# Kernel optimization log

Hardware: AMD Instinct MI355X
Metric: run time of the kernel (lower is better)

The kernel has to match this reference:

```python
import jax, jax.numpy as jnp
import numpy as np
from jax import lax


def conv2d(x, w, b=None, stride=1, pad=0):
    y = lax.conv_general_dilated(x, w, (stride, stride), [(pad, pad), (pad, pad)],
                                 dimension_numbers=('NCHW', 'OIHW', 'NCHW'))
    if b is not None:
        y = y + b[None, :, None, None]
    return y


def bilinear_resize_ac(S, Ho, Wo):
    # F.interpolate(..., mode='bilinear', align_corners=True)
    B, C, H, W = S.shape
    ys = jnp.linspace(0.0, H - 1.0, Ho)
    xs = jnp.linspace(0.0, W - 1.0, Wo)
    y0 = jnp.floor(ys).astype(jnp.int32); y1 = jnp.minimum(y0 + 1, H - 1); wy = ys - y0
    x0 = jnp.floor(xs).astype(jnp.int32); x1 = jnp.minimum(x0 + 1, W - 1); wx = xs - x0
    Sy = S[:, :, y0, :] * (1 - wy)[None, None, :, None] + S[:, :, y1, :] * wy[None, None, :, None]
    return Sy[:, :, :, x0] * (1 - wx)[None, None, None, :] + Sy[:, :, :, x1] * wx[None, None, None, :]


def deform_conv(x, offset, weight, bias=None, mask=None, stride=1, pad=1, dil=1):
    # (Modulated) deformable conv, deformable_groups=1; DCNv2 semantics:
    # offset channels are (dy, dx) pairs per kernel tap; zero padding outside.
    B, C, H, W = x.shape
    O, Ci, kh, kw = weight.shape
    K = kh * kw
    Ho, Wo = offset.shape[2], offset.shape[3]
    off = offset.reshape(B, K, 2, Ho, Wo)
    kyy, kxx = jnp.meshgrid(jnp.arange(kh) * dil, jnp.arange(kw) * dil, indexing='ij')
    kyy = kyy.reshape(K).astype(x.dtype); kxx = kxx.reshape(K).astype(x.dtype)
    base_y = (jnp.arange(Ho) * stride - pad).astype(x.dtype)
    base_x = (jnp.arange(Wo) * stride - pad).astype(x.dtype)
    py = base_y[None, None, :, None] + kyy[None, :, None, None] + off[:, :, 0]  # [B,K,Ho,Wo]
    px = base_x[None, None, None, :] + kxx[None, :, None, None] + off[:, :, 1]
    y0 = jnp.floor(py); x0 = jnp.floor(px)
    dy = py - y0; dx = px - x0
    y0i = y0.astype(jnp.int32); x0i = x0.astype(jnp.int32)
    xf = x.reshape(B, C, H * W)

    def corner(yi, xi, w):
        valid = (yi >= 0) & (yi <= H - 1) & (xi >= 0) & (xi <= W - 1)
        yc = jnp.clip(yi, 0, H - 1); xc = jnp.clip(xi, 0, W - 1)
        idx = (yc * W + xc).reshape(B, -1)  # [B, K*Ho*Wo]
        g = jax.vmap(lambda f, i: f[:, i])(xf, idx)  # [B, C, K*Ho*Wo]
        g = g.reshape(B, C, K, Ho, Wo)
        return g * (w * valid.astype(x.dtype))[:, None]

    s = (corner(y0i, x0i, (1 - dy) * (1 - dx))
         + corner(y0i, x0i + 1, (1 - dy) * dx)
         + corner(y0i + 1, x0i, dy * (1 - dx))
         + corner(y0i + 1, x0i + 1, dy * dx))  # [B,C,K,Ho,Wo]
    if mask is not None:
        s = s * mask[:, None]  # [B,1,K,Ho,Wo]
    out = jnp.einsum('bckhw,ock->bohw', s, weight.reshape(O, Ci, K))
    if bias is not None:
        out = out + bias[None, :, None, None]
    return out


def setup_inputs():
    key = jax.random.key(0)
    ks = jax.random.split(key, 16)
    B, Cin, Cout, H, W = 8, 256, 256, 64, 64

    def n(k, shape, s):
        return jax.random.normal(k, shape, jnp.float32) * s

    return {
        'x': jax.random.normal(ks[0], (B, Cin, H, W), jnp.float32),
        'S': jax.random.normal(ks[1], (B, 3, 128, 128), jnp.float32),
        'sp_w1': n(ks[2], (64, 3, 3, 3), 0.2), 'sp_b1': jnp.zeros(64), 'sp_s1': jnp.ones(64) + n(ks[3], (64,), 0.05), 'sp_o1': n(ks[3], (64,), 0.05),
        'sp_w2': n(ks[4], (64, 64, 3, 3), 0.05), 'sp_b2': jnp.zeros(64), 'sp_s2': jnp.ones(64) + n(ks[5], (64,), 0.05), 'sp_o2': n(ks[5], (64,), 0.05),
        'sp_w3': n(ks[6], (64, 64, 3, 3), 0.05), 'sp_b3': jnp.zeros(64), 'sp_s3': jnp.ones(64) + n(ks[7], (64,), 0.05), 'sp_o3': n(ks[7], (64,), 0.05),
        'off_w': n(ks[8], (18, 64, 3, 3), 0.05), 'off_b': jnp.zeros(18),
        'dc_off_w': n(ks[9], (18, 64, 3, 3), 0.05), 'dc_off_b': jnp.zeros(18),
        'dc_w': n(ks[10], (64, 64, 3, 3), 0.04),
        'm_w': n(ks[11], (9, 64, 1, 1), 0.1), 'm_b': jnp.zeros(9),
        'weight': n(ks[12], (Cout, Cin, 3, 3), 0.02), 'bias': jnp.zeros(Cout),
    }


def reference(x, S, sp_w1, sp_b1, sp_s1, sp_o1, sp_w2, sp_b2, sp_s2, sp_o2,
              sp_w3, sp_b3, sp_s3, sp_o3, off_w, off_b, dc_off_w, dc_off_b,
              dc_w, m_w, m_b, weight, bias):
    H, W = x.shape[2], x.shape[3]
    Si = bilinear_resize_ac(S, H, W)
    h = jax.nn.relu(conv2d(Si, sp_w1, sp_b1, 1, 1) * sp_s1[None, :, None, None] + sp_o1[None, :, None, None])
    h = jax.nn.relu(conv2d(h, sp_w2, sp_b2, 1, 1) * sp_s2[None, :, None, None] + sp_o2[None, :, None, None])
    h = jax.nn.relu(conv2d(h, sp_w3, sp_b3, 1, 1) * sp_s3[None, :, None, None] + sp_o3[None, :, None, None])
    offset = conv2d(h, off_w, off_b, 1, 1)                 # [B,18,H,W]
    dc_off = conv2d(h, dc_off_w, dc_off_b, 1, 1)           # internal offsets of weight_generator1 (DCNv1)
    feat = deform_conv(h, dc_off, dc_w, None, None, 1, 1, 1)
    mask = jax.nn.sigmoid(conv2d(feat, m_w, m_b, 1, 0))    # [B,9,H,W]
    return deform_conv(x, offset, weight, bias, mask, 1, 1, 1)
```

## Files before the change

kernel.cpp:

```cpp
#include <hip/hip_runtime.h>
#include <hip/hip_bf16.h>

typedef unsigned short u16;
typedef unsigned int u32;
typedef __attribute__((ext_vector_type(8))) short short8;
typedef __attribute__((ext_vector_type(4))) unsigned short ush4;
typedef __attribute__((ext_vector_type(16))) float f32x16;

#define OXT   0
#define OSI   (OXT + 8388608)
#define OA    (OSI + 98304)
#define OB    (OA + 2097152)
#define OC    (OB + 2097152)
#define OOFFS (OC + 2097152)
#define OMSK  (OOFFS + 1179648)
#define OWT   (OMSK + 294912)
#define OWSP1 (OWT + 589824)
#define OBSP1 (OWSP1 + 1728)
#define OWSP2 (OBSP1 + 64)
#define OBSP2 (OWSP2 + 36864)
#define OWSP3 (OBSP2 + 64)
#define OBSP3 (OWSP3 + 36864)
#define OWOFF (OBSP3 + 64)
#define OBOFF (OWOFF + 36864)
#define OWDC  (OBOFF + 64)

__device__ __forceinline__ u16 f2bf(float f) {
    __hip_bfloat16 hb = __float2bfloat16(f);
    return __builtin_bit_cast(u16, hb);
}
__device__ __forceinline__ float bf2f(u16 v) {
    return __builtin_bit_cast(float, (u32)v << 16);
}
__device__ __forceinline__ int sswz(int kg, int px) {
    return (px & ~7) | ((px ^ kg) & 7);
}

__device__ __forceinline__ void corner_tab_big(
    int tap, int pix0, int b, int gp,
    const float* __restrict__ offs, const float* __restrict__ maskb,
    int* car, float* cwr)
{
    int pix = pix0 + gp; int pib = pix & 4095;
    int y = pib >> 6, x = pib & 63;
    float offy = offs[(size_t)pix * 36 + tap * 2];
    float offx = offs[(size_t)pix * 36 + tap * 2 + 1];
    float m = maskb[(size_t)pix * 9 + tap];
    float py = (float)(y - 1 + tap / 3) + offy;
    float pxf = (float)(x - 1 + (tap % 3)) + offx;
    float fy = floorf(py), fx = floorf(pxf);
    int y0 = (int)fy, x0 = (int)fx;
    float dyf = py - fy, dxf = pxf - fx;
    #pragma unroll
    for (int j = 0; j < 4; j++) {
        float wj = ((j >> 1) ? dyf : 1.f - dyf) * ((j & 1) ? dxf : 1.f - dxf);
        int yy = y0 + (j >> 1), xx = x0 + (j & 1);
        bool valid = (yy >= 0 && yy < 64 && xx >= 0 && xx < 64);
        int yc = min(max(yy, 0), 63), xc = min(max(xx, 0), 63);
        car[j] = (b * 4096 + yc * 64 + xc) << 8;
        cwr[j] = valid ? wj * m : 0.f;
    }
}

__global__ __launch_bounds__(256) void prologue_k(
    const float* __restrict__ weight,
    const float* __restrict__ sp_w1, const float* __restrict__ sp_s1,
    const float* __restrict__ sp_w2, const float* __restrict__ sp_s2,
    const float* __restrict__ sp_w3, const float* __restrict__ sp_s3,
    const float* __restrict__ off_w, const float* __restrict__ dc_off_w,
    const float* __restrict__ dc_w,
    const float* __restrict__ sp_b1, const float* __restrict__ sp_o1,
    const float* __restrict__ sp_b2, const float* __restrict__ sp_o2,
    const float* __restrict__ sp_b3, const float* __restrict__ sp_o3,
    const float* __restrict__ off_b, const float* __restrict__ dc_off_b,
    const float* __restrict__ x, const float* __restrict__ S,
    float* __restrict__ ws)
{
    __shared__ float tile[64][65];
    int blk = blockIdx.x;
    int t = threadIdx.x;

    if (blk >= 4936) {
        int i = (blk - 4936) * 256 + t;
        if (i >= 8 * 64 * 64 * 3) return;
        int c = i % 3; int xq = (i / 3) & 63; int y = (i / 192) & 63; int b = i / 12288;
        const float sc = 127.0f / 63.0f;
        float sy = y * sc, sx = xq * sc;
        float fy = floorf(sy), fx = floorf(sx);
        int y0 = (int)fy, x0 = (int)fx;
        int y1 = min(y0 + 1, 127), x1 = min(x0 + 1, 127);
        float wy = sy - fy, wx = sx - fx;
        const float* Sb = S + (size_t)(b * 3 + c) * 16384;
        float v00 = Sb[y0 * 128 + x0], v01 = Sb[y0 * 128 + x1];
        float v10 = Sb[y1 * 128 + x0], v11 = Sb[y1 * 128 + x1];
        (ws + OSI)[i] = (v00 * (1.f - wy) + v10 * wy) * (1.f - wx)
                      + (v01 * (1.f - wy) + v11 * wy) * wx;
        return;
    }
    if (blk >= 2888) {
        int bb = blk - 2888;
        int chunk = bb & 3; int by = bb >> 2;
        int b = by >> 6; int y = by & 63;
        int c0 = chunk * 64;
        u16* xT = (u16*)(ws + OXT);
        for (int i = t; i < 4096; i += 256) {
            int ci = i >> 6, xi = i & 63;
            tile[ci][xi] = x[((b * 256 + c0 + ci) * 64 + y) * 64 + xi];
        }
        __syncthreads();
        for (int i = t; i < 4096; i += 256) {
            int xi = i >> 6, ci = i & 63;
            xT[((b * 64 + y) * 64 + xi) * 256 + c0 + ci] = f2bf(tile[ci][xi]);
        }
        return;
    }
    int i = blk * 256 + t;
    if (i < 589824) {
        int j = i & 7; int o = (i >> 3) & 255; int kg = i >> 11;
        int K = kg * 8 + j; int k = K >> 8; int c = K & 255;
        ((u16*)(ws + OWT))[i] = f2bf(weight[o * 2304 + c * 9 + k]);
        return;
    }
    i -= 589824;
    if (i < 1728) {
        int o = i & 63; int kc = i >> 6; int c = kc % 3; int k = kc / 3;
        ws[OWSP1 + i] = sp_w1[(o * 3 + c) * 9 + k] * sp_s1[o];
        return;
    }
    i -= 1728;
    if (i < 36864) {
        int e = i & 7; int o = (i >> 3) & 63; int kg = (i >> 9) & 7; int tp = i >> 12;
        ((u16*)(ws + OWSP2))[i] = f2bf(sp_w2[(o * 64 + kg * 8 + e) * 9 + tp] * sp_s2[o]);
        return;
    }
    i -= 36864;
    if (i < 36864) {
        int e = i & 7; int o = (i >> 3) & 63; int kg = (i >> 9) & 7; int tp = i >> 12;
        ((u16*)(ws + OWSP3))[i] = f2bf(sp_w3[(o * 64 + kg * 8 + e) * 9 + tp] * sp_s3[o]);
        return;
    }
    i -= 36864;
    if (i < 36864) {
        int e = i & 7; int o = (i >> 3) & 63; int kg = (i >> 9) & 7; int tp = i >> 12;
        int c = kg * 8 + e;
        float v = 0.f;
        if (o < 18) v = off_w[(o * 64 + c) * 9 + tp];
        else if (o < 36) v = dc_off_w[((o - 18) * 64 + c) * 9 + tp];
        ((u16*)(ws + OWOFF))[i] = f2bf(v);
        return;
    }
    i -= 36864;
    if (i < 36864) {
        int e = i & 7; int o = (i >> 3) & 63; int kg = (i >> 9) & 7; int tp = i >> 12;
        ((u16*)(ws + OWDC))[i] = f2bf(dc_w[(o * 64 + kg * 8 + e) * 9 + tp]);
        return;
    }
    i -= 36864;
    if (i < 64) { ws[OBSP1 + i] = sp_b1[i] * sp_s1[i] + sp_o1[i]; return; }
    i -= 64;
    if (i < 64) { ws[OBSP2 + i] = sp_b2[i] * sp_s2[i] + sp_o2[i]; return; }
    i -= 64;
    if (i < 64) { ws[OBSP3 + i] = sp_b3[i] * sp_s3[i] + sp_o3[i]; return; }
    i -= 64;
    if (i < 64) { ws[OBOFF + i] = (i < 18) ? off_b[i] : (i < 36 ? dc_off_b[i - 18] : 0.f); return; }
}

__global__ __launch_bounds__(256) void conv_in_k(const float* __restrict__ in,
                                                 const float* __restrict__ wt,
                                                 const float* __restrict__ bias,
                                                 u16* __restrict__ out)
{
    __shared__ float rows[3][66][3];
    int by = blockIdx.x; int b = by >> 6; int y = by & 63;
    int t = threadIdx.x;
    for (int i = t; i < 3 * 66 * 3; i += 256) {
        int r = i / 198; int rem = i - r * 198;
        int xi = rem / 3; int c = rem - xi * 3;
        int yy = y - 1 + r, xx = xi - 1;
        float v = 0.f;
        if (yy >= 0 && yy < 64 && xx >= 0 && xx < 64)
            v = in[(((b * 64 + yy) * 64 + xx) * 3) + c];
        rows[r][xi][c] = v;
    }
    __syncthreads();
    int o4 = (t & 15) * 4; int xg = t >> 4;
    float acc[4][4];
    #pragma unroll
    for (int oi = 0; oi < 4; oi++) {
        float bv = bias[o4 + oi];
        #pragma unroll
        for (int xi = 0; xi < 4; xi++) acc[oi][xi] = bv;
    }
    for (int k = 0; k < 9; k++) {
        int dy = k / 3, dx = k - 3 * (k / 3);
        for (int c = 0; c < 3; c++) {
            float4 w = *reinterpret_cast<const float4*>(&wt[(k * 3 + c) * 64 + o4]);
            #pragma unroll
            for (int xi = 0; xi < 4; xi++) {
                float iv = rows[dy][xg * 4 + xi + dx][c];
                acc[0][xi] = fmaf(w.x, iv, acc[0][xi]);
                acc[1][xi] = fmaf(w.y, iv, acc[1][xi]);
                acc[2][xi] = fmaf(w.z, iv, acc[2][xi]);
                acc[3][xi] = fmaf(w.w, iv, acc[3][xi]);
            }
        }
    }
    #pragma unroll
    for (int xi = 0; xi < 4; xi++) {
        int x = xg * 4 + xi;
        ush4 v;
        v.x = f2bf(fmaxf(acc[0][xi], 0.f));
        v.y = f2bf(fmaxf(acc[1][xi], 0.f));
        v.z = f2bf(fmaxf(acc[2][xi], 0.f));
        v.w = f2bf(fmaxf(acc[3][xi], 0.f));
        *reinterpret_cast<ush4*>(&out[((size_t)(by * 64 + x)) * 64 + o4]) = v;
    }
}

template <int MODE, bool RELU>
__global__ __launch_bounds__(256) void conv_mfma_k(const u16* __restrict__ in,
                                                   const u16* __restrict__ wm,
                                                   const float* __restrict__ bias,
                                                   u16* __restrict__ outH,
                                                   float* __restrict__ outF)
{
    __shared__ __attribute__((aligned(16))) char lds_h[3 * 66 * 128];
    __shared__ __attribute__((aligned(16))) u16 wtap[2][8][64][8];

    int t = threadIdx.x;
    int b = blockIdx.x >> 6; int y = blockIdx.x & 63;
    int pix0 = b * 4096 + y * 64;
    int wid = t >> 6, lane = t & 63;
    int lrow = lane & 31, lhi = lane >> 5;
    int o0 = (wid & 1) << 5;
    int px0 = (wid >> 1) << 5;
    int px = px0 + lrow;

    for (int i = t; i < 3 * 66 * 8; i += 256) {
        int r = i / 528; int rem = i - r * 528;
        int xi = rem >> 3; int g = rem & 7;
        int yy = y - 1 + r, xx = xi - 1;
        short8 v = {0,0,0,0,0,0,0,0};
        if (yy >= 0 && yy < 64 && xx >= 0 && xx < 64)
            v = *reinterpret_cast<const short8*>(&in[(size_t)((b * 4096 + yy * 64 + xx)) * 64 + g * 8]);
        int byte = (r * 66 + xi) * 128 + ((g * 16) ^ ((xi & 7) << 4));
        *reinterpret_cast<short8*>(lds_h + byte) = v;
    }
    {
        const char* gb = (const char*)(wm);
        char* lb = (char*)&wtap[0][0][0][0];
        #pragma unroll
        for (int i = 0; i < 2; i++) {
            int off = i * 4096 + wid * 1024;
            __builtin_amdgcn_global_load_lds(
                (const __attribute__((address_space(1))) void*)(gb + off + lane * 16),
                (__attribute__((address_space(3))) void*)(lb + off), 16, 0, 0);
        }
    }
    __syncthreads();

    f32x16 acc;
    #pragma unroll
    for (int r = 0; r < 16; r++) acc[r] = 0.f;

    #pragma unroll
    for (int tap = 0; tap < 9; tap++) {
        int cur = tap & 1, nxt = cur ^ 1;
        if (tap < 8) {
            const char* gb = (const char*)(wm + (size_t)(tap + 1) * 4096);
            char* lb = (char*)&wtap[nxt][0][0][0];
            #pragma unroll
            for (int i = 0; i < 2; i++) {
                int off = i * 4096 + wid * 1024;
                __builtin_amdgcn_global_load_lds(
                    (const __attribute__((address_space(1))) void*)(gb + off + lane * 16),
                    (__attribute__((address_space(3))) void*)(lb + off), 16, 0, 0);
            }
        }
        int dy = tap / 3, dx = tap - 3 * (tap / 3);
        int xi = px + dx;
        int rowbyte = (dy * 66 + xi) * 128;
        int swz = (xi & 7) << 4;
        #pragma unroll
        for (int ks = 0; ks < 4; ks++) {
            int kg = ks * 2 + lhi;
            short8 a0 = *reinterpret_cast<const short8*>(&wtap[cur][kg][o0 + lrow][0]);
            short8 b0 = *reinterpret_cast<const short8*>(lds_h + rowbyte + ((kg * 16) ^ swz));
            acc = __builtin_amdgcn_mfma_f32_32x32x16_bf16(a0, b0, acc, 0, 0, 0);
        }
        if (tap < 8) asm volatile("s_waitcnt vmcnt(0)" ::: "memory");
        __builtin_amdgcn_s_barrier();
    }
    __syncthreads();

    if (MODE == 0) {
        #pragma unroll
        for (int q = 0; q < 4; q++) {
            int ob = o0 + q * 8 + 4 * lhi;
            #pragma unroll
            for (int h = 0; h < 2; h++) {
                float v0 = acc[q * 4 + h * 2] + bias[ob + h * 2];
                float v1 = acc[q * 4 + h * 2 + 1] + bias[ob + h * 2 + 1];
                if (RELU) { v0 = fmaxf(v0, 0.f); v1 = fmaxf(v1, 0.f); }
                u32 pk = (u32)f2bf(v0) | ((u32)f2bf(v1) << 16);
                int byte = px * 128 + (((ob + h * 2) * 2) ^ ((px & 7) << 4));
                *reinterpret_cast<u32*>(lds_h + byte) = pk;
            }
        }
        __syncthreads();
        #pragma unroll
        for (int i = 0; i < 2; i++) {
            int cid = i * 256 + t;
            int p = cid >> 3, g = cid & 7;
            short8 v = *reinterpret_cast<const short8*>(lds_h + p * 128 + ((g * 16) ^ ((p & 7) << 4)));
            *reinterpret_cast<short8*>(&outH[(size_t)(pix0 + p) * 64 + g * 8]) = v;
        }
    } else {
        float* ltf = (float*)lds_h;
        #pragma unroll
        for (int r = 0; r < 16; r++) {
            int o = o0 + (r & 3) + ((r >> 2) << 3) + (lhi << 2);
            if (o < 36) ltf[px * 40 + o] = acc[r] + bias[o];
        }
        __syncthreads();
        for (int i = t; i < 576; i += 256) {
            int p = i / 9, q = i - 9 * (i / 9);
            float4 v = *reinterpret_cast<const float4*>(&ltf[p * 40 + q * 4]);
            *reinterpret_cast<float4*>(&outF[(size_t)(pix0 + p) * 36 + q * 4]) = v;
        }
    }
}

__global__ __launch_bounds__(512) void dconv_small_mfma(
    const u16* __restrict__ h, const float* __restrict__ offs,
    const u16* __restrict__ wdc, const float* __restrict__ m_w,
    const float* __restrict__ m_b, float* __restrict__ maskb)
{
    __shared__ __attribute__((aligned(16))) char smem[49152];
    u16 (*wtile)[8][64][8]  = (u16 (*)[8][64][8])smem;
    u16 (*stile)[8][128][8] = (u16 (*)[8][128][8])(smem + 16384);

    int t = threadIdx.x;
    int id = blockIdx.x;
    int blk = (id & 7) * 32 + (id >> 3);
    int pix0 = blk * 128;
    int b = pix0 >> 12;
    int wid = t >> 6, lane = t & 63;
    int lrow = lane & 31, lhi = lane >> 5;
    int o0 = (wid & 1) << 5;
    int px0 = (wid >> 1) << 5;
    int gp = t >> 2, gsub = t & 3;

    {
        const char* gb = (const char*)wdc;
        char* lb = (char*)&wtile[0][0][0][0];
        __builtin_amdgcn_global_load_lds(
            (const __attribute__((address_space(1))) void*)(gb + wid * 1024 + lane * 16),
            (__attribute__((address_space(3))) void*)(lb + wid * 1024), 16, 0, 0);
    }

    f32x16 acc;
    #pragma unroll
    for (int r = 0; r < 16; r++) acc[r] = 0.f;

    int car[4]; float cwr[4];

    for (int tap = 0; tap < 9; ++tap) {
        int cur = tap & 1, nxt = cur ^ 1;
        {
            int pix = pix0 + gp; int pib = pix & 4095;
            int y = pib >> 6, x = pib & 63;
            float offy = offs[(size_t)pix * 36 + 18 + tap * 2];
            float offx = offs[(size_t)pix * 36 + 18 + tap * 2 + 1];
            float py = (float)(y - 1 + tap / 3) + offy;
            float pxf = (float)(x - 1 + (tap % 3)) + offx;
            float fy = floorf(py), fx = floorf(pxf);
            int y0 = (int)fy, x0 = (int)fx;
            float dyf = py - fy, dxf = pxf - fx;
            #pragma unroll
            for (int j = 0; j < 4; j++) {
                float wj = ((j >> 1) ? dyf : 1.f - dyf) * ((j & 1) ? dxf : 1.f - dxf);
                int yy = y0 + (j >> 1), xx = x0 + (j & 1);
                bool valid = (yy >= 0 && yy < 64 && xx >= 0 && xx < 64);
                int yc = min(max(yy, 0), 63), xc = min(max(xx, 0), 63);
                car[j] = (b * 4096 + yc * 64 + xc) << 6;
                cwr[j] = valid ? wj : 0.f;
            }
        }
        int c = gsub << 4;
        float va[16];
        #pragma unroll
        for (int e = 0; e < 16; e++) va[e] = 0.f;
        #pragma unroll
        for (int j = 0; j < 4; j++) {
            float w = cwr[j];
            const u16* p = h + car[j] + c;
            short8 r0 = *reinterpret_cast<const short8*>(p);
            short8 r1 = *reinterpret_cast<const short8*>(p + 8);
            #pragma unroll
            for (int e = 0; e < 8; e++) {
                va[e]     = fmaf(w, bf2f((u16)r0[e]), va[e]);
                va[8 + e] = fmaf(w, bf2f((u16)r1[e]), va[8 + e]);
            }
        }
        short8 s0, s1;
        #pragma unroll
        for (int e = 0; e < 8; e++) { s0[e] = (short)f2bf(va[e]); s1[e] = (short)f2bf(va[8 + e]); }
        int kg0 = gsub * 2, kg1 = gsub * 2 + 1;
        *reinterpret_cast<short8*>(&stile[cur][kg0][sswz(kg0, gp)][0]) = s0;
        *reinterpret_cast<short8*>(&stile[cur][kg1][sswz(kg1, gp)][0]) = s1;

        asm volatile("s_waitcnt vmcnt(0) lgkmcnt(0)" ::: "memory");
        __builtin_amdgcn_s_barrier();

        #pragma unroll
        for (int ks = 0; ks < 4; ks++) {
            int kg = ks * 2 + lhi;
            short8 a0 = *reinterpret_cast<const short8*>(&wtile[cur][kg][o0 + lrow][0]);
            short8 b0 = *reinterpret_cast<const short8*>(&stile[cur][kg][sswz(kg, px0 + lrow)][0]);
            acc = __builtin_amdgcn_mfma_f32_32x32x16_bf16(a0, b0, acc, 0, 0, 0);
        }
        if (tap < 8) {
            const char* gb = (const char*)(wdc + (size_t)(tap + 1) * 4096);
            char* lb = (char*)&wtile[nxt][0][0][0];
            __builtin_amdgcn_global_load_lds(
                (const __attribute__((address_space(1))) void*)(gb + wid * 1024 + lane * 16),
                (__attribute__((address_space(3))) void*)(lb + wid * 1024), 16, 0, 0);
        }
    }

    __syncthreads();
    float* featl = (float*)smem;
    int pxl = px0 + lrow;
    #pragma unroll
    for (int r = 0; r < 16; r++) {
        int o = o0 + (r & 3) + ((r >> 2) << 3) + (lhi << 2);
        featl[pxl * 65 + o] = acc[r];
    }
    __syncthreads();
    if (t < 256) {
        int p = t >> 1, hh = t & 1;
        int pix = pix0 + p;
        const float* fr = &featl[p * 65];
        int j0 = hh ? 4 : 0, j1 = hh ? 9 : 4;
        for (int j = j0; j < j1; j++) {
            float a = m_b[j];
            #pragma unroll 8
            for (int cc = 0; cc < 64; cc++) a = fmaf(fr[cc], m_w[j * 64 + cc], a);
            maskb[(size_t)pix * 9 + j] = 1.f / (1.f + expf(-a));
        }
    }
}

__global__ __launch_bounds__(512) void dconv_big_mfma(
    const u16* __restrict__ xT, const float* __restrict__ offs,
    const float* __restrict__ maskb, const u16* __restrict__ wKg,
    const float* __restrict__ bias, float* __restrict__ out)
{
    __shared__ __attribute__((aligned(16))) u16 wtile[2][8][256][8];
    __shared__ __attribute__((aligned(16))) u16 stile[2][8][128][8];

    int t = threadIdx.x;
    int id = blockIdx.x;
    int blk = (id & 7) * 32 + (id >> 3);
    int pix0 = blk * 128;
    int b = pix0 >> 12, pib0 = pix0 & 4095;
    int wid = t >> 6, lane = t & 63;
    int lrow = lane & 31, lhi = lane >> 5;
    int o0 = (wid & 3) << 6;
    int px0 = (wid >> 2) << 6;
    int gp = t >> 2, gsub = t & 3;

    int car[4]; float cwr[4];
    short8 g[8];

    corner_tab_big(0, pix0, b, gp, offs, maskb, car, cwr);
    {
        int c = gsub << 4;
        #pragma unroll
        for (int j = 0; j < 4; j++) {
            const u16* p = xT + car[j] + c;
            g[j * 2]     = *reinterpret_cast<const short8*>(p);
            g[j * 2 + 1] = *reinterpret_cast<const short8*>(p + 8);
        }
    }
    {
        const char* gb = (const char*)wKg;
        char* lb = (char*)&wtile[0][0][0][0];
        #pragma unroll
        for (int i = 0; i < 4; i++) {
            int off = i * 8192 + wid * 1024;
            __builtin_amdgcn_global_load_lds(
                (const __attribute__((address_space(1))) void*)(gb + off + lane * 16),
                (__attribute__((address_space(3))) void*)(lb + off), 16, 0, 0);
        }
    }

    f32x16 acc[2][2];
    #pragma unroll
    for (int ao = 0; ao < 2; ao++)
        #pragma unroll
        for (int bp = 0; bp < 2; bp++)
            #pragma unroll
            for (int r = 0; r < 16; r++) acc[ao][bp][r] = 0.f;

    for (int kt = 0; kt < 36; ++kt) {
        int cur = kt & 1, nxt = cur ^ 1;

        float va[16];
        #pragma unroll
        for (int e = 0; e < 16; e++) va[e] = 0.f;
        #pragma unroll
        for (int j = 0; j < 4; j++) {
            float w = cwr[j];
            #pragma unroll
            for (int e = 0; e < 8; e++) {
                va[e]     = fmaf(w, bf2f((u16)g[j * 2][e]), va[e]);
                va[8 + e] = fmaf(w, bf2f((u16)g[j * 2 + 1][e]), va[8 + e]);
            }
        }
        short8 s0, s1;
        #pragma unroll
        for (int e = 0; e < 8; e++) { s0[e] = (short)f2bf(va[e]); s1[e] = (short)f2bf(va[8 + e]); }
        int kg0 = gsub * 2, kg1 = gsub * 2 + 1;
        *reinterpret_cast<short8*>(&stile[cur][kg0][sswz(kg0, gp)][0]) = s0;
        *reinterpret_cast<short8*>(&stile[cur][kg1][sswz(kg1, gp)][0]) = s1;

        if (kt < 35) {
            if (((kt + 1) & 3) == 0)
                corner_tab_big((kt + 1) >> 2, pix0, b, gp, offs, maskb, car, cwr);
            int c = (((kt + 1) & 3) << 6) + (gsub << 4);
            #pragma unroll
            for (int j = 0; j < 4; j++) {
                const u16* p = xT + car[j] + c;
                g[j * 2]     = *reinterpret_cast<const short8*>(p);
                g[j * 2 + 1] = *reinterpret_cast<const short8*>(p + 8);
            }
            asm volatile("s_waitcnt vmcnt(8) lgkmcnt(0)" ::: "memory");
        } else {
            asm volatile("s_waitcnt vmcnt(0) lgkmcnt(0)" ::: "memory");
        }
        __builtin_amdgcn_s_barrier();

        #pragma unroll
        for (int ks = 0; ks < 4; ks++) {
            int kg = ks * 2 + lhi;
            short8 a0 = *reinterpret_cast<const short8*>(&wtile[cur][kg][o0 + lrow][0]);
            short8 a1 = *reinterpret_cast<const short8*>(&wtile[cur][kg][o0 + 32 + lrow][0]);
            short8 b0 = *reinterpret_cast<const short8*>(&stile[cur][kg][sswz(kg, px0 + lrow)][0]);
            short8 b1 = *reinterpret_cast<const short8*>(&stile[cur][kg][sswz(kg, px0 + 32 + lrow)][0]);
            acc[0][0] = __builtin_amdgcn_mfma_f32_32x32x16_bf16(a0, b0, acc[0][0], 0, 0, 0);
            acc[0][1] = __builtin_amdgcn_mfma_f32_32x32x16_bf16(a0, b1, acc[0][1], 0, 0, 0);
            acc[1][0] = __builtin_amdgcn_mfma_f32_32x32x16_bf16(a1, b0, acc[1][0], 0, 0, 0);
            acc[1][1] = __builtin_amdgcn_mfma_f32_32x32x16_bf16(a1, b1, acc[1][1], 0, 0, 0);
        }
        if (kt < 35) {
            const char* gb = (const char*)(wKg + (size_t)(kt + 1) * 16384);
            char* lb = (char*)&wtile[nxt][0][0][0];
            #pragma unroll
            for (int i = 0; i < 4; i++) {
                int off = i * 8192 + wid * 1024;
                __builtin_amdgcn_global_load_lds(
                    (const __attribute__((address_space(1))) void*)(gb + off + lane * 16),
                    (__attribute__((address_space(3))) void*)(lb + off), 16, 0, 0);
            }
        }
    }

    #pragma unroll
    for (int ao = 0; ao < 2; ao++) {
        #pragma unroll
        for (int r = 0; r < 16; r++) {
            int o = o0 + ao * 32 + (r & 3) + ((r >> 2) << 3) + (lhi << 2);
            float bv = bias[o];
            size_t rowoff = ((size_t)(b * 256 + o) << 12) + pib0 + px0;
            out[rowoff + lrow] = acc[ao][0][r] + bv;
            out[rowoff + 32 + lrow] = acc[ao][1][r] + bv;
        }
    }
}

extern "C" void kernel_launch(void* const* d_in, const int* in_sizes, int n_in,
                              void* d_out, int out_size, void* d_ws, size_t ws_size,
                              hipStream_t stream)
{
    const float* x        = (const float*)d_in[0];
    const float* S        = (const float*)d_in[1];
    const float* sp_w1    = (const float*)d_in[2];
    const float* sp_b1    = (const float*)d_in[3];
    const float* sp_s1    = (const float*)d_in[4];
    const float* sp_o1    = (const float*)d_in[5];
    const float* sp_w2    = (const float*)d_in[6];
    const float* sp_b2    = (const float*)d_in[7];
    const float* sp_s2    = (const float*)d_in[8];
    const float* sp_o2    = (const float*)d_in[9];
    const float* sp_w3    = (const float*)d_in[10];
    const float* sp_b3    = (const float*)d_in[11];
    const float* sp_s3    = (const float*)d_in[12];
    const float* sp_o3    = (const float*)d_in[13];
    const float* off_w    = (const float*)d_in[14];
    const float* off_b    = (const float*)d_in[15];
    const float* dc_off_w = (const float*)d_in[16];
    const float* dc_off_b = (const float*)d_in[17];
    const float* dc_w     = (const float*)d_in[18];
    const float* m_w      = (const float*)d_in[19];
    const float* m_b      = (const float*)d_in[20];
    const float* weight   = (const float*)d_in[21];
    const float* bias     = (const float*)d_in[22];
    float* out = (float*)d_out;
    float* ws  = (float*)d_ws;

    u16*   xTb   = (u16*)(ws + OXT);
    float* Si    = ws + OSI;
    u16*   h1    = (u16*)(ws + OA);
    u16*   h2    = (u16*)(ws + OB);
    u16*   h3    = (u16*)(ws + OC);
    float* offsb = ws + OOFFS;
    float* maskb = ws + OMSK;

    prologue_k<<<5320, 256, 0, stream>>>(weight, sp_w1, sp_s1, sp_w2, sp_s2,
                                         sp_w3, sp_s3, off_w, dc_off_w, dc_w,
                                         sp_b1, sp_o1, sp_b2, sp_o2, sp_b3, sp_o3,
                                         off_b, dc_off_b, x, S, ws);
    conv_in_k<<<512, 256, 0, stream>>>(Si, ws + OWSP1, ws + OBSP1, h1);
    conv_mfma_k<0, true><<<512, 256, 0, stream>>>(h1, (const u16*)(ws + OWSP2),
                                                  ws + OBSP2, h2, nullptr);
    conv_mfma_k<0, true><<<512, 256, 0, stream>>>(h2, (const u16*)(ws + OWSP3),
                                                  ws + OBSP3, h3, nullptr);
    conv_mfma_k<1, false><<<512, 256, 0, stream>>>(h3, (const u16*)(ws + OWOFF),
                                                   ws + OBOFF, nullptr, offsb);
    dconv_small_mfma<<<256, 512, 0, stream>>>(h3, offsb, (const u16*)(ws + OWDC),
                                              m_w, m_b, maskb);
    dconv_big_mfma<<<256, 512, 0, stream>>>(xTb, offsb, maskb,
                                            (const u16*)(ws + OWT), bias, out);
}
```

Measured before the change: 132.0 us.

## Prefetch gathers across taps, triple-buffer conv weights, halve big deform-conv pixel tile

conv_mfma_k now keeps three weight-tap buffers and prefetches two taps ahead, waiting with a partial vmcnt so a weight load overlaps more compute. dconv_small_mfma computes the next tap's corner table and issues its bilinear gathers before the barrier, so gather latency overlaps the current tap's MFMAs. dconv_big_mfma shrinks each block's pixel tile from 128 to 64, launches twice as many blocks, and gives each wave 32 outputs by 64 pixels with fewer registers. The aim is better latency hiding and occupancy, at the cost of more LDS in the conv kernel and more weight-tile reloads across the extra blocks.

```diff
diff --git a/kernel.cpp b/kernel.cpp
--- a/kernel.cpp
+++ b/kernel.cpp
@@ -62,6 +62,30 @@
     }
 }
 
+__device__ __forceinline__ void corner_tab_small(
+    int tap, int pix0, int b, int gp,
+    const float* __restrict__ offs, int* car, float* cwr)
+{
+    int pix = pix0 + gp; int pib = pix & 4095;
+    int y = pib >> 6, x = pib & 63;
+    float offy = offs[(size_t)pix * 36 + 18 + tap * 2];
+    float offx = offs[(size_t)pix * 36 + 18 + tap * 2 + 1];
+    float py = (float)(y - 1 + tap / 3) + offy;
+    float pxf = (float)(x - 1 + (tap % 3)) + offx;
+    float fy = floorf(py), fx = floorf(pxf);
+    int y0 = (int)fy, x0 = (int)fx;
+    float dyf = py - fy, dxf = pxf - fx;
+    #pragma unroll
+    for (int j = 0; j < 4; j++) {
+        float wj = ((j >> 1) ? dyf : 1.f - dyf) * ((j & 1) ? dxf : 1.f - dxf);
+        int yy = y0 + (j >> 1), xx = x0 + (j & 1);
+        bool valid = (yy >= 0 && yy < 64 && xx >= 0 && xx < 64);
+        int yc = min(max(yy, 0), 63), xc = min(max(xx, 0), 63);
+        car[j] = (b * 4096 + yc * 64 + xc) << 6;
+        cwr[j] = valid ? wj : 0.f;
+    }
+}
+
 __global__ __launch_bounds__(256) void prologue_k(
     const float* __restrict__ weight,
     const float* __restrict__ sp_w1, const float* __restrict__ sp_s1,
@@ -225,7 +249,7 @@
                                                    float* __restrict__ outF)
 {
     __shared__ __attribute__((aligned(16))) char lds_h[3 * 66 * 128];
-    __shared__ __attribute__((aligned(16))) u16 wtap[2][8][64][8];
+    __shared__ __attribute__((aligned(16))) u16 wtap[3][8][64][8];
 
     int t = threadIdx.x;
     int b = blockIdx.x >> 6; int y = blockIdx.x & 63;
@@ -246,9 +270,10 @@
         int byte = (r * 66 + xi) * 128 + ((g * 16) ^ ((xi & 7) << 4));
         *reinterpret_cast<short8*>(lds_h + byte) = v;
     }
-    {
-        const char* gb = (const char*)(wm);
-        char* lb = (char*)&wtap[0][0][0][0];
+    #pragma unroll
+    for (int p = 0; p < 2; p++) {
+        const char* gb = (const char*)(wm + (size_t)p * 4096);
+        char* lb = (char*)&wtap[p][0][0][0];
         #pragma unroll
         for (int i = 0; i < 2; i++) {
             int off = i * 4096 + wid * 1024;
@@ -265,10 +290,11 @@
 
     #pragma unroll
     for (int tap = 0; tap < 9; tap++) {
-        int cur = tap & 1, nxt = cur ^ 1;
-        if (tap < 8) {
-            const char* gb = (const char*)(wm + (size_t)(tap + 1) * 4096);
-            char* lb = (char*)&wtap[nxt][0][0][0];
+        int cur = tap % 3;
+        if (tap < 7) {
+            int nb = (tap + 2) % 3;
+            const char* gb = (const char*)(wm + (size_t)(tap + 2) * 4096);
+            char* lb = (char*)&wtap[nb][0][0][0];
             #pragma unroll
             for (int i = 0; i < 2; i++) {
                 int off = i * 4096 + wid * 1024;
@@ -288,8 +314,11 @@
             short8 b0 = *reinterpret_cast<const short8*>(lds_h + rowbyte + ((kg * 16) ^ swz));
             acc = __builtin_amdgcn_mfma_f32_32x32x16_bf16(a0, b0, acc, 0, 0, 0);
         }
-        if (tap < 8) asm volatile("s_waitcnt vmcnt(0)" ::: "memory");
-        __builtin_amdgcn_s_barrier();
+        if (tap < 8) {
+            if (tap < 7) asm volatile("s_waitcnt vmcnt(2)" ::: "memory");
+            else         asm volatile("s_waitcnt vmcnt(0)" ::: "memory");
+            __builtin_amdgcn_s_barrier();
+        }
     }
     __syncthreads();
 
@@ -351,6 +380,19 @@
     int px0 = (wid >> 1) << 5;
     int gp = t >> 2, gsub = t & 3;
 
+    int car[4]; float cwr[4];
+    short8 g[8];
+
+    corner_tab_small(0, pix0, b, gp, offs, car, cwr);
+    {
+        int c = gsub << 4;
+        #pragma unroll
+        for (int j = 0; j < 4; j++) {
+            const u16* p = h + car[j] + c;
+            g[j * 2]     = *reinterpret_cast<const short8*>(p);
+            g[j * 2 + 1] = *reinterpret_cast<const short8*>(p + 8);
+        }
+    }
     {
         const char* gb = (const char*)wdc;
         char* lb = (char*)&wtile[0][0][0][0];
@@ -363,44 +405,19 @@
     #pragma unroll
     for (int r = 0; r < 16; r++) acc[r] = 0.f;
 
-    int car[4]; float cwr[4];
-
     for (int tap = 0; tap < 9; ++tap) {
         int cur = tap & 1, nxt = cur ^ 1;
-        {
-            int pix = pix0 + gp; int pib = pix & 4095;
-            int y = pib >> 6, x = pib & 63;
-            float offy = offs[(size_t)pix * 36 + 18 + tap * 2];
-            float offx = offs[(size_t)pix * 36 + 18 + tap * 2 + 1];
-            float py = (float)(y - 1 + tap / 3) + offy;
-            float pxf = (float)(x - 1 + (tap % 3)) + offx;
-            float fy = floorf(py), fx = floorf(pxf);
-            int y0 = (int)fy, x0 = (int)fx;
-            float dyf = py - fy, dxf = pxf - fx;
-            #pragma unroll
-            for (int j = 0; j < 4; j++) {
-                float wj = ((j >> 1) ? dyf : 1.f - dyf) * ((j & 1) ? dxf : 1.f - dxf);
-                int yy = y0 + (j >> 1), xx = x0 + (j & 1);
-                bool valid = (yy >= 0 && yy < 64 && xx >= 0 && xx < 64);
-                int yc = min(max(yy, 0), 63), xc = min(max(xx, 0), 63);
-                car[j] = (b * 4096 + yc * 64 + xc) << 6;
-                cwr[j] = valid ? wj : 0.f;
-            }
-        }
-        int c = gsub << 4;
+
         float va[16];
         #pragma unroll
         for (int e = 0; e < 16; e++) va[e] = 0.f;
         #pragma unroll
         for (int j = 0; j < 4; j++) {
             float w = cwr[j];
-            const u16* p = h + car[j] + c;
-            short8 r0 = *reinterpret_cast<const short8*>(p);
-            short8 r1 = *reinterpret_cast<const short8*>(p + 8);
             #pragma unroll
             for (int e = 0; e < 8; e++) {
-                va[e]     = fmaf(w, bf2f((u16)r0[e]), va[e]);
-                va[8 + e] = fmaf(w, bf2f((u16)r1[e]), va[8 + e]);
+                va[e]     = fmaf(w, bf2f((u16)g[j * 2][e]), va[e]);
+                va[8 + e] = fmaf(w, bf2f((u16)g[j * 2 + 1][e]), va[8 + e]);
             }
         }
         short8 s0, s1;
@@ -410,7 +427,19 @@
         *reinterpret_cast<short8*>(&stile[cur][kg0][sswz(kg0, gp)][0]) = s0;
         *reinterpret_cast<short8*>(&stile[cur][kg1][sswz(kg1, gp)][0]) = s1;
 
-        asm volatile("s_waitcnt vmcnt(0) lgkmcnt(0)" ::: "memory");
+        if (tap < 8) {
+            corner_tab_small(tap + 1, pix0, b, gp, offs, car, cwr);
+            int c = gsub << 4;
+            #pragma unroll
+            for (int j = 0; j < 4; j++) {
+                const u16* p = h + car[j] + c;
+                g[j * 2]     = *reinterpret_cast<const short8*>(p);
+                g[j * 2 + 1] = *reinterpret_cast<const short8*>(p + 8);
+            }
+            asm volatile("s_waitcnt vmcnt(8) lgkmcnt(0)" ::: "memory");
+        } else {
+            asm volatile("s_waitcnt vmcnt(0) lgkmcnt(0)" ::: "memory");
+        }
         __builtin_amdgcn_s_barrier();
 
         #pragma unroll
@@ -458,31 +487,27 @@
     const float* __restrict__ bias, float* __restrict__ out)
 {
     __shared__ __attribute__((aligned(16))) u16 wtile[2][8][256][8];
-    __shared__ __attribute__((aligned(16))) u16 stile[2][8][128][8];
+    __shared__ __attribute__((aligned(16))) u16 stile[2][8][64][8];
 
     int t = threadIdx.x;
     int id = blockIdx.x;
-    int blk = (id & 7) * 32 + (id >> 3);
-    int pix0 = blk * 128;
+    int blk = (id & 7) * 64 + (id >> 3);
+    int pix0 = blk * 64;
     int b = pix0 >> 12, pib0 = pix0 & 4095;
     int wid = t >> 6, lane = t & 63;
     int lrow = lane & 31, lhi = lane >> 5;
-    int o0 = (wid & 3) << 6;
-    int px0 = (wid >> 2) << 6;
-    int gp = t >> 2, gsub = t & 3;
+    int o0 = wid << 5;
+    int gp = t >> 3, gsub = t & 7;
 
     int car[4]; float cwr[4];
-    short8 g[8];
+    short8 g[4];
 
     corner_tab_big(0, pix0, b, gp, offs, maskb, car, cwr);
     {
-        int c = gsub << 4;
-        #pragma unroll
-        for (int j = 0; j < 4; j++) {
-            const u16* p = xT + car[j] + c;
-            g[j * 2]     = *reinterpret_cast<const short8*>(p);
-            g[j * 2 + 1] = *reinterpret_cast<const short8*>(p + 8);
-        }
+        int c = gsub << 3;
+        #pragma unroll
+        for (int j = 0; j < 4; j++)
+            g[j] = *reinterpret_cast<const short8*>(xT + car[j] + c);
     }
     {
         const char* gb = (const char*)wKg;
@@ -496,47 +521,37 @@
         }
     }
 
-    f32x16 acc[2][2];
-    #pragma unroll
-    for (int ao = 0; ao < 2; ao++)
-        #pragma unroll
-        for (int bp = 0; bp < 2; bp++)
-            #pragma unroll
-            for (int r = 0; r < 16; r++) acc[ao][bp][r] = 0.f;
+    f32x16 acc[2];
+    #pragma unroll
+    for (int fp = 0; fp < 2; fp++)
+        #pragma unroll
+        for (int r = 0; r < 16; r++) acc[fp][r] = 0.f;
 
     for (int kt = 0; kt < 36; ++kt) {
         int cur = kt & 1, nxt = cur ^ 1;
 
-        float va[16];
-        #pragma unroll
-        for (int e = 0; e < 16; e++) va[e] = 0.f;
+        float va[8];
+        #pragma unroll
+        for (int e = 0; e < 8; e++) va[e] = 0.f;
         #pragma unroll
         for (int j = 0; j < 4; j++) {
             float w = cwr[j];
             #pragma unroll
-            for (int e = 0; e < 8; e++) {
-                va[e]     = fmaf(w, bf2f((u16)g[j * 2][e]), va[e]);
-                va[8 + e] = fmaf(w, bf2f((u16)g[j * 2 + 1][e]), va[8 + e]);
-            }
-        }
-        short8 s0, s1;
-        #pragma unroll
-        for (int e = 0; e < 8; e++) { s0[e] = (short)f2bf(va[e]); s1[e] = (short)f2bf(va[8 + e]); }
-        int kg0 = gsub * 2, kg1 = gsub * 2 + 1;
-        *reinterpret_cast<short8*>(&stile[cur][kg0][sswz(kg0, gp)][0]) = s0;
-        *reinterpret_cast<short8*>(&stile[cur][kg1][sswz(kg1, gp)][0]) = s1;
+            for (int e = 0; e < 8; e++) va[e] = fmaf(w, bf2f((u16)g[j][e]), va[e]);
+        }
+        short8 s0;
+        #pragma unroll
+        for (int e = 0; e < 8; e++) s0[e] = (short)f2bf(va[e]);
+        *reinterpret_cast<short8*>(&stile[cur][gsub][sswz(gsub, gp)][0]) = s0;
 
         if (kt < 35) {
             if (((kt + 1) & 3) == 0)
                 corner_tab_big((kt + 1) >> 2, pix0, b, gp, offs, maskb, car, cwr);
-            int c = (((kt + 1) & 3) << 6) + (gsub << 4);
-            #pragma unroll
-            for (int j = 0; j < 4; j++) {
-                const u16* p = xT + car[j] + c;
-                g[j * 2]     = *reinterpret_cast<const short8*>(p);
-                g[j * 2 + 1] = *reinterpret_cast<const short8*>(p + 8);
-            }
-            asm volatile("s_waitcnt vmcnt(8) lgkmcnt(0)" ::: "memory");
+            int c = (((kt + 1) & 3) << 6) + (gsub << 3);
+            #pragma unroll
+            for (int j = 0; j < 4; j++)
+                g[j] = *reinterpret_cast<const short8*>(xT + car[j] + c);
+            asm volatile("s_waitcnt vmcnt(4) lgkmcnt(0)" ::: "memory");
         } else {
             asm volatile("s_waitcnt vmcnt(0) lgkmcnt(0)" ::: "memory");
         }
@@ -546,13 +561,10 @@
         for (int ks = 0; ks < 4; ks++) {
             int kg = ks * 2 + lhi;
             short8 a0 = *reinterpret_cast<const short8*>(&wtile[cur][kg][o0 + lrow][0]);
-            short8 a1 = *reinterpret_cast<const short8*>(&wtile[cur][kg][o0 + 32 + lrow][0]);
-            short8 b0 = *reinterpret_cast<const short8*>(&stile[cur][kg][sswz(kg, px0 + lrow)][0]);
-            short8 b1 = *reinterpret_cast<const short8*>(&stile[cur][kg][sswz(kg, px0 + 32 + lrow)][0]);
-            acc[0][0] = __builtin_amdgcn_mfma_f32_32x32x16_bf16(a0, b0, acc[0][0], 0, 0, 0);
-            acc[0][1] = __builtin_amdgcn_mfma_f32_32x32x16_bf16(a0, b1, acc[0][1], 0, 0, 0);
-            acc[1][0] = __builtin_amdgcn_mfma_f32_32x32x16_bf16(a1, b0, acc[1][0], 0, 0, 0);
-            acc[1][1] = __builtin_amdgcn_mfma_f32_32x32x16_bf16(a1, b1, acc[1][1], 0, 0, 0);
+            short8 b0 = *reinterpret_cast<const short8*>(&stile[cur][kg][sswz(kg, lrow)][0]);
+            short8 b1 = *reinterpret_cast<const short8*>(&stile[cur][kg][sswz(kg, 32 + lrow)][0]);
+            acc[0] = __builtin_amdgcn_mfma_f32_32x32x16_bf16(a0, b0, acc[0], 0, 0, 0);
+            acc[1] = __builtin_amdgcn_mfma_f32_32x32x16_bf16(a0, b1, acc[1], 0, 0, 0);
         }
         if (kt < 35) {
             const char* gb = (const char*)(wKg + (size_t)(kt + 1) * 16384);
@@ -568,14 +580,12 @@
     }
 
     #pragma unroll
-    for (int ao = 0; ao < 2; ao++) {
+    for (int fp = 0; fp < 2; fp++) {
         #pragma unroll
         for (int r = 0; r < 16; r++) {
-            int o = o0 + ao * 32 + (r & 3) + ((r >> 2) << 3) + (lhi << 2);
-            float bv = bias[o];
-            size_t rowoff = ((size_t)(b * 256 + o) << 12) + pib0 + px0;
-            out[rowoff + lrow] = acc[ao][0][r] + bv;
-            out[rowoff + 32 + lrow] = acc[ao][1][r] + bv;
+            int o = o0 + (r & 3) + ((r >> 2) << 3) + (lhi << 2);
+            size_t rowoff = ((size_t)(b * 256 + o) << 12) + pib0;
+            out[rowoff + fp * 32 + lrow] = acc[fp][r] + bias[o];
         }
     }
 }
@@ -631,6 +641,6 @@
                                                    ws + OBOFF, nullptr, offsb);
     dconv_small_mfma<<<256, 512, 0, stream>>>(h3, offsb, (const u16*)(ws + OWDC),
                                               m_w, m_b, maskb);
-    dconv_big_mfma<<<256, 512, 0, stream>>>(xTb, offsb, maskb,
+    dconv_big_mfma<<<512, 512, 0, stream>>>(xTb, offsb, maskb,
                                             (const u16*)(ws + OWT), bias, out);
 }
```

After: 137.6 us. +4.2%, slower.

## Preload all conv tap weights to LDS, double rows per block, prefetch deform gathers

Applied to the files above, without the earlier changes.

The 3x3 MFMA conv kernels now load all nine taps' weights into LDS up front, which removes the per-tap double-buffered weight loads and barriers. Each block now covers two output rows with 512 threads, so grid size halves. The small deformable conv likewise preloads all tap weights and software-pipelines the bilinear corner gathers, issuing the next tap's global loads before the MFMA of the current tap. The cost is much larger LDS per block, around 104KB in the small deform kernel, which reduces occupancy. The extra register-held gather data also adds pressure.

```diff
diff --git a/kernel.cpp b/kernel.cpp
--- a/kernel.cpp
+++ b/kernel.cpp
@@ -62,6 +62,30 @@
     }
 }
 
+__device__ __forceinline__ void corner_tab_small(
+    int tap, int pix0, int b, int gp,
+    const float* __restrict__ offs, int* car, float* cwr)
+{
+    int pix = pix0 + gp; int pib = pix & 4095;
+    int y = pib >> 6, x = pib & 63;
+    float offy = offs[(size_t)pix * 36 + 18 + tap * 2];
+    float offx = offs[(size_t)pix * 36 + 18 + tap * 2 + 1];
+    float py = (float)(y - 1 + tap / 3) + offy;
+    float pxf = (float)(x - 1 + (tap % 3)) + offx;
+    float fy = floorf(py), fx = floorf(pxf);
+    int y0 = (int)fy, x0 = (int)fx;
+    float dyf = py - fy, dxf = pxf - fx;
+    #pragma unroll
+    for (int j = 0; j < 4; j++) {
+        float wj = ((j >> 1) ? dyf : 1.f - dyf) * ((j & 1) ? dxf : 1.f - dxf);
+        int yy = y0 + (j >> 1), xx = x0 + (j & 1);
+        bool valid = (yy >= 0 && yy < 64 && xx >= 0 && xx < 64);
+        int yc = min(max(yy, 0), 63), xc = min(max(xx, 0), 63);
+        car[j] = (b * 4096 + yc * 64 + xc) << 6;
+        cwr[j] = valid ? wj : 0.f;
+    }
+}
+
 __global__ __launch_bounds__(256) void prologue_k(
     const float* __restrict__ weight,
     const float* __restrict__ sp_w1, const float* __restrict__ sp_s1,
@@ -218,28 +242,29 @@
 }
 
 template <int MODE, bool RELU>
-__global__ __launch_bounds__(256) void conv_mfma_k(const u16* __restrict__ in,
+__global__ __launch_bounds__(512) void conv_mfma_k(const u16* __restrict__ in,
                                                    const u16* __restrict__ wm,
                                                    const float* __restrict__ bias,
                                                    u16* __restrict__ outH,
                                                    float* __restrict__ outF)
 {
-    __shared__ __attribute__((aligned(16))) char lds_h[3 * 66 * 128];
-    __shared__ __attribute__((aligned(16))) u16 wtap[2][8][64][8];
+    __shared__ __attribute__((aligned(16))) char lds_h[4 * 66 * 128];
+    __shared__ __attribute__((aligned(16))) u16 wtap[9][8][64][8];
 
     int t = threadIdx.x;
-    int b = blockIdx.x >> 6; int y = blockIdx.x & 63;
-    int pix0 = b * 4096 + y * 64;
+    int b = blockIdx.x >> 5; int y0 = (blockIdx.x & 31) * 2;
+    int pix0 = b * 4096 + y0 * 64;
     int wid = t >> 6, lane = t & 63;
     int lrow = lane & 31, lhi = lane >> 5;
     int o0 = (wid & 1) << 5;
     int px0 = (wid >> 1) << 5;
     int px = px0 + lrow;
-
-    for (int i = t; i < 3 * 66 * 8; i += 256) {
+    int ry_l = px >> 6, xc = px & 63;
+
+    for (int i = t; i < 4 * 66 * 8; i += 512) {
         int r = i / 528; int rem = i - r * 528;
         int xi = rem >> 3; int g = rem & 7;
-        int yy = y - 1 + r, xx = xi - 1;
+        int yy = y0 - 1 + r, xx = xi - 1;
         short8 v = {0,0,0,0,0,0,0,0};
         if (yy >= 0 && yy < 64 && xx >= 0 && xx < 64)
             v = *reinterpret_cast<const short8*>(&in[(size_t)((b * 4096 + yy * 64 + xx)) * 64 + g * 8]);
@@ -247,11 +272,11 @@
         *reinterpret_cast<short8*>(lds_h + byte) = v;
     }
     {
-        const char* gb = (const char*)(wm);
+        const char* gb = (const char*)wm;
         char* lb = (char*)&wtap[0][0][0][0];
         #pragma unroll
-        for (int i = 0; i < 2; i++) {
-            int off = i * 4096 + wid * 1024;
+        for (int i = 0; i < 9; i++) {
+            int off = i * 8192 + wid * 1024;
             __builtin_amdgcn_global_load_lds(
                 (const __attribute__((address_space(1))) void*)(gb + off + lane * 16),
                 (__attribute__((address_space(3))) void*)(lb + off), 16, 0, 0);
@@ -265,31 +290,17 @@
 
     #pragma unroll
     for (int tap = 0; tap < 9; tap++) {
-        int cur = tap & 1, nxt = cur ^ 1;
-        if (tap < 8) {
-            const char* gb = (const char*)(wm + (size_t)(tap + 1) * 4096);
-            char* lb = (char*)&wtap[nxt][0][0][0];
-            #pragma unroll
-            for (int i = 0; i < 2; i++) {
-                int off = i * 4096 + wid * 1024;
-                __builtin_amdgcn_global_load_lds(
-                    (const __attribute__((address_space(1))) void*)(gb + off + lane * 16),
-                    (__attribute__((address_space(3))) void*)(lb + off), 16, 0, 0);
-            }
-        }
         int dy = tap / 3, dx = tap - 3 * (tap / 3);
-        int xi = px + dx;
-        int rowbyte = (dy * 66 + xi) * 128;
+        int xi = xc + dx;
+        int rowbyte = ((ry_l + dy) * 66 + xi) * 128;
         int swz = (xi & 7) << 4;
         #pragma unroll
         for (int ks = 0; ks < 4; ks++) {
             int kg = ks * 2 + lhi;
-            short8 a0 = *reinterpret_cast<const short8*>(&wtap[cur][kg][o0 + lrow][0]);
+            short8 a0 = *reinterpret_cast<const short8*>(&wtap[tap][kg][o0 + lrow][0]);
             short8 b0 = *reinterpret_cast<const short8*>(lds_h + rowbyte + ((kg * 16) ^ swz));
             acc = __builtin_amdgcn_mfma_f32_32x32x16_bf16(a0, b0, acc, 0, 0, 0);
         }
-        if (tap < 8) asm volatile("s_waitcnt vmcnt(0)" ::: "memory");
-        __builtin_amdgcn_s_barrier();
     }
     __syncthreads();
 
@@ -310,7 +321,7 @@
         __syncthreads();
         #pragma unroll
         for (int i = 0; i < 2; i++) {
-            int cid = i * 256 + t;
+            int cid = i * 512 + t;
             int p = cid >> 3, g = cid & 7;
             short8 v = *reinterpret_cast<const short8*>(lds_h + p * 128 + ((g * 16) ^ ((p & 7) << 4)));
             *reinterpret_cast<short8*>(&outH[(size_t)(pix0 + p) * 64 + g * 8]) = v;
@@ -323,7 +334,7 @@
             if (o < 36) ltf[px * 40 + o] = acc[r] + bias[o];
         }
         __syncthreads();
-        for (int i = t; i < 576; i += 256) {
+        for (int i = t; i < 1152; i += 512) {
             int p = i / 9, q = i - 9 * (i / 9);
             float4 v = *reinterpret_cast<const float4*>(&ltf[p * 40 + q * 4]);
             *reinterpret_cast<float4*>(&outF[(size_t)(pix0 + p) * 36 + q * 4]) = v;
@@ -336,9 +347,9 @@
     const u16* __restrict__ wdc, const float* __restrict__ m_w,
     const float* __restrict__ m_b, float* __restrict__ maskb)
 {
-    __shared__ __attribute__((aligned(16))) char smem[49152];
+    __shared__ __attribute__((aligned(16))) char smem[106496];
     u16 (*wtile)[8][64][8]  = (u16 (*)[8][64][8])smem;
-    u16 (*stile)[8][128][8] = (u16 (*)[8][128][8])(smem + 16384);
+    u16 (*stile)[8][128][8] = (u16 (*)[8][128][8])(smem + 73728);
 
     int t = threadIdx.x;
     int id = blockIdx.x;
@@ -351,56 +362,49 @@
     int px0 = (wid >> 1) << 5;
     int gp = t >> 2, gsub = t & 3;
 
+    int car[4]; float cwr[4];
+    short8 g[8];
+
+    corner_tab_small(0, pix0, b, gp, offs, car, cwr);
+    {
+        int c = gsub << 4;
+        #pragma unroll
+        for (int j = 0; j < 4; j++) {
+            const u16* p = h + car[j] + c;
+            g[j * 2]     = *reinterpret_cast<const short8*>(p);
+            g[j * 2 + 1] = *reinterpret_cast<const short8*>(p + 8);
+        }
+    }
     {
         const char* gb = (const char*)wdc;
-        char* lb = (char*)&wtile[0][0][0][0];
-        __builtin_amdgcn_global_load_lds(
-            (const __attribute__((address_space(1))) void*)(gb + wid * 1024 + lane * 16),
-            (__attribute__((address_space(3))) void*)(lb + wid * 1024), 16, 0, 0);
-    }
+        char* lb = (char*)smem;
+        #pragma unroll
+        for (int i = 0; i < 9; i++) {
+            int off = i * 8192 + wid * 1024;
+            __builtin_amdgcn_global_load_lds(
+                (const __attribute__((address_space(1))) void*)(gb + off + lane * 16),
+                (__attribute__((address_space(3))) void*)(lb + off), 16, 0, 0);
+        }
+    }
+    asm volatile("s_waitcnt vmcnt(0)" ::: "memory");
 
     f32x16 acc;
     #pragma unroll
     for (int r = 0; r < 16; r++) acc[r] = 0.f;
 
-    int car[4]; float cwr[4];
-
     for (int tap = 0; tap < 9; ++tap) {
-        int cur = tap & 1, nxt = cur ^ 1;
-        {
-            int pix = pix0 + gp; int pib = pix & 4095;
-            int y = pib >> 6, x = pib & 63;
-            float offy = offs[(size_t)pix * 36 + 18 + tap * 2];
-            float offx = offs[(size_t)pix * 36 + 18 + tap * 2 + 1];
-            float py = (float)(y - 1 + tap / 3) + offy;
-            float pxf = (float)(x - 1 + (tap % 3)) + offx;
-            float fy = floorf(py), fx = floorf(pxf);
-            int y0 = (int)fy, x0 = (int)fx;
-            float dyf = py - fy, dxf = pxf - fx;
-            #pragma unroll
-            for (int j = 0; j < 4; j++) {
-                float wj = ((j >> 1) ? dyf : 1.f - dyf) * ((j & 1) ? dxf : 1.f - dxf);
-                int yy = y0 + (j >> 1), xx = x0 + (j & 1);
-                bool valid = (yy >= 0 && yy < 64 && xx >= 0 && xx < 64);
-                int yc = min(max(yy, 0), 63), xc = min(max(xx, 0), 63);
-                car[j] = (b * 4096 + yc * 64 + xc) << 6;
-                cwr[j] = valid ? wj : 0.f;
-            }
-        }
-        int c = gsub << 4;
+        int cur = tap & 1;
+
         float va[16];
         #pragma unroll
         for (int e = 0; e < 16; e++) va[e] = 0.f;
         #pragma unroll
         for (int j = 0; j < 4; j++) {
             float w = cwr[j];
-            const u16* p = h + car[j] + c;
-            short8 r0 = *reinterpret_cast<const short8*>(p);
-            short8 r1 = *reinterpret_cast<const short8*>(p + 8);
             #pragma unroll
             for (int e = 0; e < 8; e++) {
-                va[e]     = fmaf(w, bf2f((u16)r0[e]), va[e]);
-                va[8 + e] = fmaf(w, bf2f((u16)r1[e]), va[8 + e]);
+                va[e]     = fmaf(w, bf2f((u16)g[j * 2][e]), va[e]);
+                va[8 + e] = fmaf(w, bf2f((u16)g[j * 2 + 1][e]), va[8 + e]);
             }
         }
         short8 s0, s1;
@@ -410,22 +414,25 @@
         *reinterpret_cast<short8*>(&stile[cur][kg0][sswz(kg0, gp)][0]) = s0;
         *reinterpret_cast<short8*>(&stile[cur][kg1][sswz(kg1, gp)][0]) = s1;
 
-        asm volatile("s_waitcnt vmcnt(0) lgkmcnt(0)" ::: "memory");
+        if (tap < 8) {
+            corner_tab_small(tap + 1, pix0, b, gp, offs, car, cwr);
+            int c = gsub << 4;
+            #pragma unroll
+            for (int j = 0; j < 4; j++) {
+                const u16* p = h + car[j] + c;
+                g[j * 2]     = *reinterpret_cast<const short8*>(p);
+                g[j * 2 + 1] = *reinterpret_cast<const short8*>(p + 8);
+            }
+        }
+        asm volatile("s_waitcnt lgkmcnt(0)" ::: "memory");
         __builtin_amdgcn_s_barrier();
 
         #pragma unroll
         for (int ks = 0; ks < 4; ks++) {
             int kg = ks * 2 + lhi;
-            short8 a0 = *reinterpret_cast<const short8*>(&wtile[cur][kg][o0 + lrow][0]);
+            short8 a0 = *reinterpret_cast<const short8*>(&wtile[tap][kg][o0 + lrow][0]);
             short8 b0 = *reinterpret_cast<const short8*>(&stile[cur][kg][sswz(kg, px0 + lrow)][0]);
             acc = __builtin_amdgcn_mfma_f32_32x32x16_bf16(a0, b0, acc, 0, 0, 0);
-        }
-        if (tap < 8) {
-            const char* gb = (const char*)(wdc + (size_t)(tap + 1) * 4096);
-            char* lb = (char*)&wtile[nxt][0][0][0];
-            __builtin_amdgcn_global_load_lds(
-                (const __attribute__((address_space(1))) void*)(gb + wid * 1024 + lane * 16),
-                (__attribute__((address_space(3))) void*)(lb + wid * 1024), 16, 0, 0);
         }
     }
 
@@ -623,11 +630,11 @@
                                          sp_b1, sp_o1, sp_b2, sp_o2, sp_b3, sp_o3,
                                          off_b, dc_off_b, x, S, ws);
     conv_in_k<<<512, 256, 0, stream>>>(Si, ws + OWSP1, ws + OBSP1, h1);
-    conv_mfma_k<0, true><<<512, 256, 0, stream>>>(h1, (const u16*)(ws + OWSP2),
+    conv_mfma_k<0, true><<<256, 512, 0, stream>>>(h1, (const u16*)(ws + OWSP2),
                                                   ws + OBSP2, h2, nullptr);
-    conv_mfma_k<0, true><<<512, 256, 0, stream>>>(h2, (const u16*)(ws + OWSP3),
+    conv_mfma_k<0, true><<<256, 512, 0, stream>>>(h2, (const u16*)(ws + OWSP3),
                                                   ws + OBSP3, h3, nullptr);
-    conv_mfma_k<1, false><<<512, 256, 0, stream>>>(h3, (const u16*)(ws + OWOFF),
+    conv_mfma_k<1, false><<<256, 512, 0, stream>>>(h3, (const u16*)(ws + OWOFF),
                                                    ws + OBOFF, nullptr, offsb);
     dconv_small_mfma<<<256, 512, 0, stream>>>(h3, offsb, (const u16*)(ws + OWDC),
                                               m_w, m_b, maskb);
```

After: 122.5 us. 7.2% less time.
